# Performance work log

Measured on AMD Instinct MI355X. Metric: run time of the kernel, lower is better.

Reference implementation:

```python
import jax, jax.numpy as jnp
import numpy as np

B = 65536
SEM, COL, LAT, K, NL = 768, 64, 64, 256, 3
EPS_LN = 1e-5

def layernorm(x, g, b):
    m = jnp.mean(x, axis=-1, keepdims=True)
    v = jnp.mean((x - m) ** 2, axis=-1, keepdims=True)
    return (x - m) * jax.lax.rsqrt(v + EPS_LN) * g + b

def l2norm(x):
    n = jnp.sqrt(jnp.sum(x * x, axis=-1, keepdims=True))
    return x / jnp.maximum(n, 1e-12)

def setup_inputs() -> dict:
    key = jax.random.key(0)
    ks = jax.random.split(key, 32)
    g = lambda i, shape, s=0.02: jax.random.normal(ks[i], shape, jnp.float32) * s
    inp = {
        'semantic_emb': jax.random.normal(ks[0], (B, SEM), jnp.float32),
        'collab_emb':   jax.random.normal(ks[1], (B, COL), jnp.float32),
        # gate network: Linear(64,128)+LN+ReLU+Linear(128,64)+Sigmoid
        'gate_w1': g(2, (COL, 128)), 'gate_b1': jnp.zeros((128,)),
        'gate_ln_g': jnp.ones((128,)), 'gate_ln_b': jnp.zeros((128,)),
        'gate_w2': g(3, (128, COL)), 'gate_b2': jnp.zeros((COL,)),
        # fusion layernorm over 832
        'fusion_ln_g': jnp.ones((SEM + COL,)), 'fusion_ln_b': jnp.zeros((SEM + COL,)),
        # encoder (no bias): 832->512->256->128->64, SiLU between
        'enc_w1': g(4, (SEM + COL, 512)), 'enc_w2': g(5, (512, 256)),
        'enc_w3': g(6, (256, 128)),       'enc_w4': g(7, (128, LAT)),
        # shared decoder (no bias): 64->128->256->512, SiLU after each
        'dec_w1': g(8, (LAT, 128)), 'dec_w2': g(9, (128, 256)), 'dec_w3': g(10, (256, 512)),
        # semantic head: 512->1536 (+LN,ReLU) ->768
        'sem_w1': g(11, (512, 2 * SEM)), 'sem_b1': jnp.zeros((2 * SEM,)),
        'sem_ln_g': jnp.ones((2 * SEM,)), 'sem_ln_b': jnp.zeros((2 * SEM,)),
        'sem_w2': g(12, (2 * SEM, SEM)), 'sem_b2': jnp.zeros((SEM,)),
        # collab head: 512->256 (+LN,ReLU) ->64
        'col_w1': g(13, (512, 256)), 'col_b1': jnp.zeros((256,)),
        'col_ln_g': jnp.ones((256,)), 'col_ln_b': jnp.zeros((256,)),
        'col_w2': g(14, (256, COL)), 'col_b2': jnp.zeros((COL,)),
        # residual codebooks [n_layers, n_embed, latent_dim]
        'codebooks': jax.random.normal(ks[15], (NL, K, LAT), jnp.float32),
    }
    return inp

def _forward(semantic_emb, collab_emb, gate_w1, gate_b1, gate_ln_g, gate_ln_b,
             gate_w2, gate_b2, fusion_ln_g, fusion_ln_b,
             enc_w1, enc_w2, enc_w3, enc_w4, dec_w1, dec_w2, dec_w3,
             sem_w1, sem_b1, sem_ln_g, sem_ln_b, sem_w2, sem_b2,
             col_w1, col_b1, col_ln_g, col_ln_b, col_w2, col_b2, codebooks):
    # --- gated fusion (dropout inactive at eval) ---
    h = jax.nn.relu(layernorm(collab_emb @ gate_w1 + gate_b1, gate_ln_g, gate_ln_b))
    gate_values = jax.nn.sigmoid(h @ gate_w2 + gate_b2)
    denoised_collab = gate_values * collab_emb
    fused = layernorm(jnp.concatenate([semantic_emb, denoised_collab], axis=-1),
                      fusion_ln_g, fusion_ln_b)
    # --- encoder MLP ---
    z = jax.nn.silu(fused @ enc_w1)
    z = jax.nn.silu(z @ enc_w2)
    z = jax.nn.silu(z @ enc_w3)
    z = z @ enc_w4  # [B, LAT]
    # --- residual quantization (eval: nearest-neighbor, straight-through) ---
    residual = z
    z_q_total = jnp.zeros_like(z)
    cb_loss = jnp.float32(0.0)
    cm_loss = jnp.float32(0.0)
    codes_list = []
    for l in range(NL):
        residual = l2norm(residual)  # normalize_residuals=True
        cb = codebooks[l]  # [K, LAT]
        # argmin ||r - e||^2 == argmax (r.e - 0.5||e||^2)
        score = residual @ cb.T - 0.5 * jnp.sum(cb * cb, axis=-1)
        codes = jnp.argmax(score, axis=-1)  # [B]
        e = cb[codes]  # [B, LAT]
        cb_loss = cb_loss + jnp.mean((e - jax.lax.stop_gradient(residual)) ** 2)
        cm_loss = cm_loss + jnp.mean((jax.lax.stop_gradient(e) - residual) ** 2)
        z_q_layer = residual + jax.lax.stop_gradient(e - residual)  # straight-through
        z_q_total = z_q_total + z_q_layer
        residual = residual - z_q_layer
        codes_list.append(codes)
    codes = jnp.stack(codes_list, axis=1)  # [B, NL]
    # --- dual decoders ---
    s = jax.nn.silu(z_q_total @ dec_w1)
    s = jax.nn.silu(s @ dec_w2)
    s = jax.nn.silu(s @ dec_w3)  # [B, 512]
    sh = jax.nn.relu(layernorm(s @ sem_w1 + sem_b1, sem_ln_g, sem_ln_b))
    semantic_recon = sh @ sem_w2 + sem_b2
    ch = jax.nn.relu(layernorm(s @ col_w1 + col_b1, col_ln_g, col_ln_b))
    collab_recon = ch @ col_w2 + col_b2
    return semantic_recon, collab_recon, z_q_total, codes, cb_loss, cm_loss, gate_values

def reference(semantic_emb, collab_emb, gate_w1, gate_b1, gate_ln_g, gate_ln_b,
              gate_w2, gate_b2, fusion_ln_g, fusion_ln_b,
              enc_w1, enc_w2, enc_w3, enc_w4, dec_w1, dec_w2, dec_w3,
              sem_w1, sem_b1, sem_ln_g, sem_ln_b, sem_w2, sem_b2,
              col_w1, col_b1, col_ln_g, col_ln_b, col_w2, col_b2, codebooks):
    return _forward(semantic_emb, collab_emb, gate_w1, gate_b1, gate_ln_g, gate_ln_b,
                    gate_w2, gate_b2, fusion_ln_g, fusion_ln_b,
                    enc_w1, enc_w2, enc_w3, enc_w4, dec_w1, dec_w2, dec_w3,
                    sem_w1, sem_b1, sem_ln_g, sem_ln_b, sem_w2, sem_b2,
                    col_w1, col_b1, col_ln_g, col_ln_b, col_w2, col_b2, codebooks)
```

## Files before the change

### kernel.cpp

```cpp
#include <hip/hip_runtime.h>
#include <hip/hip_bf16.h>
#include <math.h>

typedef __bf16 bf16;
typedef __attribute__((ext_vector_type(8))) __bf16 v8bf;
typedef __attribute__((ext_vector_type(4))) float v4f;
typedef _Float16 f16;
typedef __attribute__((ext_vector_type(8))) _Float16 v8h;
typedef __attribute__((ext_vector_type(4))) _Float16 v4h;

__device__ __forceinline__ void xcd_swizzle(int& bm, int& bn) {
  const int nx = gridDim.x;
  const int id = blockIdx.y * nx + blockIdx.x;
  const int slot = id >> 3;
  const int row_in = slot / nx;
  const int bmi = (id & 7) * (gridDim.y >> 3) + row_in;
  const int bni = slot - row_in * nx;
  bm = bmi << 7; bn = bni << 7;
}

__device__ __forceinline__ void xcd_swizzle256(int& bm, int& bn) {
  const int nx = gridDim.x;
  const int id = blockIdx.y * nx + blockIdx.x;
  const int slot = id >> 3;
  const int row_in = slot / nx;
  const int bmi = (id & 7) * (gridDim.y >> 3) + row_in;
  const int bni = slot - row_in * nx;
  bm = bmi << 8; bn = bni << 8;
}

__global__ void wconv_t(const float* __restrict__ W, bf16* __restrict__ Wt, int Kd, int Nd) {
  int e = blockIdx.x * 256 + threadIdx.x;
  if (e < Kd * Nd) {
    int k = e / Nd, n = e - k * Nd;
    Wt[n * Kd + k] = (bf16)W[e];
  }
}

__global__ void wsplit_t(const float* __restrict__ W, f16* __restrict__ W0,
                         f16* __restrict__ W1, int Kd, int Nd) {
  int e = blockIdx.x * 256 + threadIdx.x;
  if (e < Kd * Nd) {
    int k = e / Nd, n = e - k * Nd;
    float v = W[e] * 2048.0f;
    f16 h0 = (f16)v;
    f16 h1 = (f16)(v - (float)h0);
    W0[n * Kd + k] = h0;
    W1[n * Kd + k] = h1;
  }
}

__global__ void cbt_k(const float* __restrict__ cb, float* __restrict__ cbT) {
  int e = blockIdx.x * 256 + threadIdx.x;
  if (e < 3 * 256 * 64) {
    int l = e >> 14, rem = e & 16383;
    int c = rem >> 6, d = rem & 63;
    cbT[l * 16384 + d * 256 + c] = cb[e];
  }
}

__global__ void nhn_k(const float* __restrict__ cb, float* __restrict__ nhn) {
  int l = blockIdx.x, c = threadIdx.x;
  const float* p = cb + l * 16384 + c * 64;
  double s = 0.0;
  for (int d = 0; d < 64; ++d) { double v = (double)p[d]; s += v * v; }
  nhn[l * 256 + c] = (float)(-0.5 * s);
}

template <int EPI>
__global__ __launch_bounds__(256, 2) void sgemm128(
    const float* __restrict__ A, const float* __restrict__ W,
    const float* __restrict__ bias, const float* __restrict__ lng,
    const float* __restrict__ lnb, float* __restrict__ C, int N, int Kd) {
  __shared__ float As[32][132];
  __shared__ float Bs[32][128];
  const int tid = threadIdx.x;
  const int w = tid >> 6, l = tid & 63;
  int tx, ty;
  if (EPI == 2) { tx = tid & 15; ty = tid >> 4; }
  else { tx = ((w & 1) << 3) | (l & 7); ty = ((w >> 1) << 3) | (l >> 3); }
  int bm, bn;
  xcd_swizzle(bm, bn);

  float acc[8][8];
#pragma unroll
  for (int i = 0; i < 8; ++i)
#pragma unroll
    for (int j = 0; j < 8; ++j) acc[i][j] = 0.0f;

  for (int k0 = 0; k0 < Kd; k0 += 32) {
    __syncthreads();
#pragma unroll
    for (int jj = 0; jj < 4; ++jj) {
      int p = tid + 256 * jj;
      int arow = p >> 3, aks = (p & 7) << 2;
      float4 v = *(const float4*)(A + (size_t)(bm + arow) * Kd + k0 + aks);
      As[aks][arow] = v.x; As[aks + 1][arow] = v.y;
      As[aks + 2][arow] = v.z; As[aks + 3][arow] = v.w;
      int bk = p >> 5, bns = (p & 31) << 2;
      float4 u = *(const float4*)(W + (size_t)(k0 + bk) * N + bn + bns);
      *(float4*)(&Bs[bk][bns]) = u;
    }
    __syncthreads();
    float cacc[8][8];
#pragma unroll
    for (int i = 0; i < 8; ++i)
#pragma unroll
      for (int j = 0; j < 8; ++j) cacc[i][j] = 0.0f;
#pragma unroll 4
    for (int kk = 0; kk < 32; ++kk) {
      float a[8], b[8];
#pragma unroll
      for (int i = 0; i < 8; ++i) a[i] = As[kk][ty * 8 + i];
#pragma unroll
      for (int j = 0; j < 8; ++j) b[j] = Bs[kk][tx * 8 + j];
#pragma unroll
      for (int i = 0; i < 8; ++i)
#pragma unroll
        for (int j = 0; j < 8; ++j) cacc[i][j] = fmaf(a[i], b[j], cacc[i][j]);
    }
#pragma unroll
    for (int i = 0; i < 8; ++i)
#pragma unroll
      for (int j = 0; j < 8; ++j) acc[i][j] += cacc[i][j];
  }

  const int colb = bn + tx * 8;
  if (EPI == 0) {
#pragma unroll
    for (int i = 0; i < 8; ++i) {
      int row = bm + ty * 8 + i;
      float o[8];
#pragma unroll
      for (int j = 0; j < 8; ++j) { float v = acc[i][j]; o[j] = v / (1.0f + expf(-v)); }
      *(float4*)(C + (size_t)row * N + colb) = make_float4(o[0], o[1], o[2], o[3]);
      *(float4*)(C + (size_t)row * N + colb + 4) = make_float4(o[4], o[5], o[6], o[7]);
    }
  } else if (EPI == 1) {
    float bb[8];
#pragma unroll
    for (int j = 0; j < 8; ++j) bb[j] = bias[colb + j];
#pragma unroll
    for (int i = 0; i < 8; ++i) {
      int row = bm + ty * 8 + i;
      float o[8];
#pragma unroll
      for (int j = 0; j < 8; ++j) o[j] = acc[i][j] + bb[j];
      *(float4*)(C + (size_t)row * N + colb) = make_float4(o[0], o[1], o[2], o[3]);
      *(float4*)(C + (size_t)row * N + colb + 4) = make_float4(o[4], o[5], o[6], o[7]);
    }
  } else {
    float bb[8], lg[8], lb[8];
#pragma unroll
    for (int j = 0; j < 8; ++j) { bb[j] = bias[colb + j]; lg[j] = lng[colb + j]; lb[j] = lnb[colb + j]; }
#pragma unroll
    for (int i = 0; i < 8; ++i) {
      int row = bm + ty * 8 + i;
      float v[8]; float s = 0.0f;
#pragma unroll
      for (int j = 0; j < 8; ++j) { v[j] = acc[i][j] + bb[j]; s += v[j]; }
      s += __shfl_xor(s, 1); s += __shfl_xor(s, 2); s += __shfl_xor(s, 4); s += __shfl_xor(s, 8);
      float mean = s * (1.0f / 128.0f);
      float ss = 0.0f;
#pragma unroll
      for (int j = 0; j < 8; ++j) { float t = v[j] - mean; ss += t * t; }
      ss += __shfl_xor(ss, 1); ss += __shfl_xor(ss, 2); ss += __shfl_xor(ss, 4); ss += __shfl_xor(ss, 8);
      float rs = 1.0f / sqrtf(ss * (1.0f / 128.0f) + 1e-5f);
      float o[8];
#pragma unroll
      for (int j = 0; j < 8; ++j) o[j] = fmaxf((v[j] - mean) * rs * lg[j] + lb[j], 0.0f);
      *(float4*)(C + (size_t)row * N + colb) = make_float4(o[0], o[1], o[2], o[3]);
      *(float4*)(C + (size_t)row * N + colb + 4) = make_float4(o[4], o[5], o[6], o[7]);
    }
  }
}

template <int EPI>
__global__ __launch_bounds__(256, 2) void sgemm64(
    const float* __restrict__ A, const float* __restrict__ W,
    const float* __restrict__ bias, const float* __restrict__ aux,
    float* __restrict__ C, float* __restrict__ C2, int Kd) {
  __shared__ float As[32][132];
  __shared__ float Bs[32][64];
  const int tid = threadIdx.x;
  const int tx = tid & 15, ty = tid >> 4;
  const int bm = blockIdx.x << 7;

  float acc[8][4];
#pragma unroll
  for (int i = 0; i < 8; ++i)
#pragma unroll
    for (int j = 0; j < 4; ++j) acc[i][j] = 0.0f;

  for (int k0 = 0; k0 < Kd; k0 += 32) {
    __syncthreads();
#pragma unroll
    for (int jj = 0; jj < 4; ++jj) {
      int p = tid + 256 * jj;
      int arow = p >> 3, aks = (p & 7) << 2;
      float4 v = *(const float4*)(A + (size_t)(bm + arow) * Kd + k0 + aks);
      As[aks][arow] = v.x; As[aks + 1][arow] = v.y;
      As[aks + 2][arow] = v.z; As[aks + 3][arow] = v.w;
    }
#pragma unroll
    for (int jj = 0; jj < 2; ++jj) {
      int p = tid + 256 * jj;
      int bk = p >> 4, bns = (p & 15) << 2;
      float4 u = *(const float4*)(W + (size_t)(k0 + bk) * 64 + bns);
      *(float4*)(&Bs[bk][bns]) = u;
    }
    __syncthreads();
    float cacc[8][4];
#pragma unroll
    for (int i = 0; i < 8; ++i)
#pragma unroll
      for (int j = 0; j < 4; ++j) cacc[i][j] = 0.0f;
#pragma unroll 4
    for (int kk = 0; kk < 32; ++kk) {
      float a[8], b[4];
#pragma unroll
      for (int i = 0; i < 8; ++i) a[i] = As[kk][ty * 8 + i];
#pragma unroll
      for (int j = 0; j < 4; ++j) b[j] = Bs[kk][tx * 4 + j];
#pragma unroll
      for (int i = 0; i < 8; ++i)
#pragma unroll
        for (int j = 0; j < 4; ++j) cacc[i][j] = fmaf(a[i], b[j], cacc[i][j]);
    }
#pragma unroll
    for (int i = 0; i < 8; ++i)
#pragma unroll
      for (int j = 0; j < 4; ++j) acc[i][j] += cacc[i][j];
  }

  const int colb = tx * 4;
  if (EPI == 0) {
#pragma unroll
    for (int i = 0; i < 8; ++i) {
      int row = bm + ty * 8 + i;
      float ss = 0.0f;
#pragma unroll
      for (int j = 0; j < 4; ++j) ss += acc[i][j] * acc[i][j];
      ss += __shfl_xor(ss, 1); ss += __shfl_xor(ss, 2); ss += __shfl_xor(ss, 4); ss += __shfl_xor(ss, 8);
      float nrm = fmaxf(sqrtf(ss), 1e-12f);
      *(float4*)(C + (size_t)row * 64 + colb) =
          make_float4(acc[i][0] / nrm, acc[i][1] / nrm, acc[i][2] / nrm, acc[i][3] / nrm);
    }
  } else if (EPI == 1) {
    float bb[4];
#pragma unroll
    for (int j = 0; j < 4; ++j) bb[j] = bias[colb + j];
#pragma unroll
    for (int i = 0; i < 8; ++i) {
      int row = bm + ty * 8 + i;
      *(float4*)(C + (size_t)row * 64 + colb) =
          make_float4(acc[i][0] + bb[0], acc[i][1] + bb[1], acc[i][2] + bb[2], acc[i][3] + bb[3]);
    }
  } else {
    float bb[4];
#pragma unroll
    for (int j = 0; j < 4; ++j) bb[j] = bias[colb + j];
#pragma unroll
    for (int i = 0; i < 8; ++i) {
      int row = bm + ty * 8 + i;
      float4 av = *(const float4*)(aux + (size_t)row * 64 + colb);
      float g[4];
#pragma unroll
      for (int j = 0; j < 4; ++j) g[j] = 1.0f / (1.0f + expf(-(acc[i][j] + bb[j])));
      *(float4*)(C + (size_t)row * 64 + colb) = make_float4(g[0], g[1], g[2], g[3]);
      *(float4*)(C2 + (size_t)row * 64 + colb) =
          make_float4(g[0] * av.x, g[1] * av.y, g[2] * av.z, g[3] * av.w);
    }
  }
}

__global__ __launch_bounds__(256) void fuse_ln(
    const float* __restrict__ sem, const float* __restrict__ den,
    const float* __restrict__ fg, const float* __restrict__ fb,
    f16* __restrict__ fA0, f16* __restrict__ fA1) {
  const int w = threadIdx.x >> 6, l = threadIdx.x & 63;
  float fgv[13], fbv[13];
#pragma unroll
  for (int q = 0; q < 12; ++q) { fgv[q] = fg[q * 64 + l]; fbv[q] = fb[q * 64 + l]; }
  fgv[12] = fg[768 + l]; fbv[12] = fb[768 + l];
  for (int it = 0; it < 4; ++it) {
    int r = (blockIdx.x * 4 + w) * 4 + it;
    float sv[12];
#pragma unroll
    for (int q = 0; q < 12; ++q) sv[q] = sem[(size_t)r * 768 + q * 64 + l];
    float dv = den[(size_t)r * 64 + l];
    float s = dv;
#pragma unroll
    for (int q = 0; q < 12; ++q) s += sv[q];
#pragma unroll
    for (int m = 1; m < 64; m <<= 1) s += __shfl_xor(s, m, 64);
    float mean = s * (1.0f / 832.0f);
    float t0 = dv - mean;
    float ss = t0 * t0;
#pragma unroll
    for (int q = 0; q < 12; ++q) { float t = sv[q] - mean; ss += t * t; }
#pragma unroll
    for (int m = 1; m < 64; m <<= 1) ss += __shfl_xor(ss, m, 64);
    float sc = 1.0f / sqrtf(ss * (1.0f / 832.0f) + 1e-5f);
#pragma unroll
    for (int q = 0; q < 13; ++q) {
      float y = (q < 12) ? ((sv[q] - mean) * sc * fgv[q] + fbv[q])
                         : (t0 * sc * fgv[12] + fbv[12]);
      float t = y * 256.0f;
      f16 h0 = (f16)t;
      size_t idx = (size_t)r * 832 + q * 64 + l;
      fA0[idx] = h0;
      fA1[idx] = (f16)(t - (float)h0);
    }
  }
}

template <int LAYER>
__global__ __launch_bounds__(256) void argupd(
    const float* __restrict__ scores, const float* __restrict__ cbl,
    float* __restrict__ rn, float* __restrict__ zq, float* __restrict__ codes,
    float* __restrict__ loss, bf16* __restrict__ zqb) {
  const int w = threadIdx.x >> 6, l = threadIdx.x & 63;
  const int base = (blockIdx.x * 4 + w) * 16;
  float lacc = 0.0f;
  for (int it = 0; it < 16; ++it) {
    int r = base + it;
    float4 s4 = *(const float4*)(scores + (size_t)r * 256 + l * 4);
    float bs = s4.x; int bi = l * 4;
    if (s4.y > bs) { bs = s4.y; bi = l * 4 + 1; }
    if (s4.z > bs) { bs = s4.z; bi = l * 4 + 2; }
    if (s4.w > bs) { bs = s4.w; bi = l * 4 + 3; }
#pragma unroll
    for (int m = 1; m < 64; m <<= 1) {
      float os = __shfl_xor(bs, m, 64);
      int oi = __shfl_xor(bi, m, 64);
      if (os > bs || (os == bs && oi < bi)) { bs = os; bi = oi; }
    }
    float e = cbl[bi * 64 + l];
    float rl = rn[(size_t)r * 64 + l];
    float emr = e - rl;
    float zql = rl + emr;
    lacc += emr * emr;
    if (l == 0) codes[r * 3 + LAYER] = (float)bi;
    if (LAYER == 0) {
      zq[(size_t)r * 64 + l] = zql;
    } else if (LAYER == 1) {
      zq[(size_t)r * 64 + l] += zql;
    } else {
      float tot = zq[(size_t)r * 64 + l] + zql;
      zq[(size_t)r * 64 + l] = tot;
      zqb[(size_t)r * 64 + l] = (bf16)tot;
    }
    if (LAYER < 2) {
      float rnew = rl - zql;
      float ss = rnew * rnew;
#pragma unroll
      for (int m = 1; m < 64; m <<= 1) ss += __shfl_xor(ss, m, 64);
      float nrm = fmaxf(sqrtf(ss), 1e-12f);
      rn[(size_t)r * 64 + l] = rnew / nrm;
    }
  }
#pragma unroll
  for (int m = 1; m < 64; m <<= 1) lacc += __shfl_xor(lacc, m, 64);
  if (l == 0) {
    float v = lacc * (1.0f / 4194304.0f);
    atomicAdd(loss, v);
    atomicAdd(loss + 1, v);
  }
}

typedef __attribute__((address_space(3))) void lds_void_t;
typedef __attribute__((address_space(1))) const void gbl_void_t;
__device__ __forceinline__ void gl_lds16(const void* g, void* l) {
  __builtin_amdgcn_global_load_lds((gbl_void_t*)g, (lds_void_t*)l, 16, 0, 0);
}

template <int EPI>
__global__ __launch_bounds__(256, 3) void bgemm(
    const bf16* __restrict__ A, const bf16* __restrict__ Wt,
    const float* __restrict__ bias, void* __restrict__ Cv, int N, int Kd) {
  __shared__ __align__(16) bf16 As[128 * 32];
  __shared__ __align__(16) bf16 Bs[128 * 32];
  const int tid = threadIdx.x;
  const int w = tid >> 6, l = tid & 63;
  int bm, bn;
  xcd_swizzle(bm, bn);
  const int wm = (w >> 1) << 6, wn = (w & 1) << 6;

  v4f acc[4][4];
  v4f z4 = {0.0f, 0.0f, 0.0f, 0.0f};
#pragma unroll
  for (int i = 0; i < 4; ++i)
#pragma unroll
    for (int j = 0; j < 4; ++j) acc[i][j] = z4;

  const int srow = (w << 5) + (l >> 2);
  const int skc = (l & 3) << 3;
  const bf16* ga0 = A + (size_t)(bm + srow) * Kd + skc;
  const bf16* gb0 = Wt + (size_t)(bn + srow) * Kd + skc;
  char* la0 = (char*)As + (w << 11);
  char* lb0 = (char*)Bs + (w << 11);

  for (int k0 = 0; k0 < Kd; k0 += 32) {
    __syncthreads();
    gl_lds16(ga0 + k0, la0);
    gl_lds16(ga0 + (size_t)16 * Kd + k0, la0 + 1024);
    gl_lds16(gb0 + k0, lb0);
    gl_lds16(gb0 + (size_t)16 * Kd + k0, lb0 + 1024);
    __syncthreads();
    v8bf af[4], bfr[4];
#pragma unroll
    for (int f = 0; f < 4; ++f) {
      af[f] = *(const v8bf*)(As + (wm + f * 16 + (l & 15)) * 32 + ((l >> 4) << 3));
      bfr[f] = *(const v8bf*)(Bs + (wn + f * 16 + (l & 15)) * 32 + ((l >> 4) << 3));
    }
#pragma unroll
    for (int mf = 0; mf < 4; ++mf)
#pragma unroll
      for (int nf = 0; nf < 4; ++nf)
        acc[mf][nf] = __builtin_amdgcn_mfma_f32_16x16x32_bf16(af[mf], bfr[nf], acc[mf][nf], 0, 0, 0);
  }

  const int cbase = bn + wn + (l & 15);
  float bb[4];
  if (EPI != 0) {
#pragma unroll
    for (int nf = 0; nf < 4; ++nf) bb[nf] = bias[cbase + nf * 16];
  }
#pragma unroll
  for (int mf = 0; mf < 4; ++mf) {
#pragma unroll
    for (int i = 0; i < 4; ++i) {
      int row = bm + wm + mf * 16 + ((l >> 4) << 2) + i;
#pragma unroll
      for (int nf = 0; nf < 4; ++nf) {
        int col = cbase + nf * 16;
        float v = acc[mf][nf][i];
        if (EPI == 0) {
          v = v / (1.0f + __expf(-v));
          ((bf16*)Cv)[(size_t)row * N + col] = (bf16)v;
        } else if (EPI == 1) {
          v += bb[nf];
          ((bf16*)Cv)[(size_t)row * N + col] = (bf16)v;
        } else {
          v += bb[nf];
          ((float*)Cv)[(size_t)row * N + col] = v;
        }
      }
    }
  }
}

__device__ __forceinline__ void stage_plane(const f16* __restrict__ src, int Kd,
                                            int rbase, int k0, char* base,
                                            int wid, int l) {
#pragma unroll
  for (int j = 0; j < 2; ++j) {
    int Cc = wid * 128 + j * 64 + l;
    int cc = Cc ^ ((Cc >> 3) & 3);
    gl_lds16(src + (size_t)(rbase + (cc >> 2)) * Kd + k0 + (cc & 3) * 8,
             base + wid * 2048 + j * 1024);
  }
}

__device__ __forceinline__ v8h ldsfragh(const char* base, int row, int kb) {
  int p = row * 64 + kb;
  p ^= ((p >> 7) & 3) << 4;
  return *(const v8h*)(base + p);
}

template <int EPI>
__global__ __launch_bounds__(256, 3) void hgemmp(
    const f16* __restrict__ A0, const f16* __restrict__ A1,
    const f16* __restrict__ W0, const f16* __restrict__ W1,
    f16* __restrict__ O0, f16* __restrict__ O1, float* __restrict__ Cf,
    int N, int Kd) {
  __shared__ __align__(16) char smem[32768];
  const int tid = threadIdx.x;
  const int w = tid >> 6, l = tid & 63;
  int bm, bn;
  xcd_swizzle(bm, bn);
  const int wm = (w >> 1) << 6, wn = (w & 1) << 6;
  const int kb = (l >> 4) << 4;

  char* pa0 = smem;
  char* pa1 = smem + 8192;
  char* pb0 = smem + 16384;
  char* pb1 = smem + 24576;

  v4f acc[4][4];
  v4f z4 = {0.0f, 0.0f, 0.0f, 0.0f};
#pragma unroll
  for (int i = 0; i < 4; ++i)
#pragma unroll
    for (int j = 0; j < 4; ++j) acc[i][j] = z4;

  for (int k0 = 0; k0 < Kd; k0 += 32) {
    __syncthreads();
    stage_plane(A0, Kd, bm, k0, pa0, w, l);
    stage_plane(A1, Kd, bm, k0, pa1, w, l);
    stage_plane(W0, Kd, bn, k0, pb0, w, l);
    stage_plane(W1, Kd, bn, k0, pb1, w, l);
    __syncthreads();
    v8h a0f[4], a1f[4], b0f[4], b1f[4];
#pragma unroll
    for (int f = 0; f < 4; ++f) {
      a0f[f] = ldsfragh(pa0, wm + f * 16 + (l & 15), kb);
      a1f[f] = ldsfragh(pa1, wm + f * 16 + (l & 15), kb);
      b0f[f] = ldsfragh(pb0, wn + f * 16 + (l & 15), kb);
      b1f[f] = ldsfragh(pb1, wn + f * 16 + (l & 15), kb);
    }
#pragma unroll
    for (int mf = 0; mf < 4; ++mf)
#pragma unroll
      for (int nf = 0; nf < 4; ++nf) {
        acc[mf][nf] = __builtin_amdgcn_mfma_f32_16x16x32_f16(a0f[mf], b1f[nf], acc[mf][nf], 0, 0, 0);
        acc[mf][nf] = __builtin_amdgcn_mfma_f32_16x16x32_f16(a1f[mf], b0f[nf], acc[mf][nf], 0, 0, 0);
        acc[mf][nf] = __builtin_amdgcn_mfma_f32_16x16x32_f16(a0f[mf], b0f[nf], acc[mf][nf], 0, 0, 0);
      }
  }

  const float sc = 1.0f / (256.0f * 2048.0f);
  const int cbase = bn + wn + (l & 15);
#pragma unroll
  for (int mf = 0; mf < 4; ++mf) {
#pragma unroll
    for (int i = 0; i < 4; ++i) {
      int row = bm + wm + mf * 16 + ((l >> 4) << 2) + i;
#pragma unroll
      for (int nf = 0; nf < 4; ++nf) {
        int col = cbase + nf * 16;
        float v = acc[mf][nf][i] * sc;
        v = v / (1.0f + expf(-v));
        if (EPI == 0) {
          float t = v * 256.0f;
          f16 h0 = (f16)t;
          O0[(size_t)row * N + col] = h0;
          O1[(size_t)row * N + col] = (f16)(t - (float)h0);
        } else {
          Cf[(size_t)row * N + col] = v;
        }
      }
    }
  }
}

__device__ __forceinline__ void stage_half(const bf16* __restrict__ src, int Kd,
                                           int rbase, int k0, char* hb8,
                                           int wid, int l) {
#pragma unroll
  for (int j = 0; j < 2; ++j) {
    int Cc = wid * 128 + j * 64 + l;
    int cc = Cc ^ (((Cc >> 3) & 3) << 1);
    gl_lds16(src + (size_t)(rbase + (cc >> 3)) * Kd + k0 + (cc & 7) * 8,
             hb8 + wid * 2048 + j * 1024);
  }
}

__device__ __forceinline__ v8bf ldsfrag(const char* base, int row, int kb) {
  int p = row * 128 + kb;
  p ^= ((p >> 7) & 3) << 5;
  return *(const v8bf*)(base + p);
}

__device__ __forceinline__ void rd_a(v8bf (&af)[2][4], const char* ab, int mh, int l) {
  const int rb = mh * 64 + (l & 15);
  const int kb = (l >> 4) * 16;
#pragma unroll
  for (int ks = 0; ks < 2; ++ks)
#pragma unroll
    for (int mf = 0; mf < 4; ++mf)
      af[ks][mf] = ldsfrag(ab, rb + mf * 16, ks * 64 + kb);
}

__device__ __forceinline__ void rd_b(v8bf (&bfr)[2][2], const char* bbp, int nh, int wl, int l) {
  const int rb = wl + nh * 32 + (l & 15);
  const int kb = (l >> 4) * 16;
#pragma unroll
  for (int ks = 0; ks < 2; ++ks)
#pragma unroll
    for (int nf = 0; nf < 2; ++nf)
      bfr[ks][nf] = ldsfrag(bbp, rb + nf * 16, ks * 64 + kb);
}

__device__ __forceinline__ void qmfma(v4f (&q)[4][2], const v8bf (&af)[2][4],
                                      const v8bf (&bfr)[2][2]) {
  __builtin_amdgcn_s_setprio(1);
#pragma unroll
  for (int ks = 0; ks < 2; ++ks)
#pragma unroll
    for (int mf = 0; mf < 4; ++mf)
#pragma unroll
      for (int nf = 0; nf < 2; ++nf)
        q[mf][nf] = __builtin_amdgcn_mfma_f32_16x16x32_bf16(af[ks][mf], bfr[ks][nf],
                                                            q[mf][nf], 0, 0, 0);
  __builtin_amdgcn_s_setprio(0);
}

#define PHASE_BAR() do { __builtin_amdgcn_s_barrier(); __builtin_amdgcn_sched_barrier(0); } while (0)

template <int EPI>
__global__ __launch_bounds__(512, 2) void bgemm8(
    const bf16* __restrict__ A, const bf16* __restrict__ Wt,
    const float* __restrict__ bias, void* __restrict__ Cv, int N, int Kd) {
  __shared__ __align__(16) char smem[131072];
  const int tid = threadIdx.x;
  const int wid = tid >> 6, l = tid & 63;
  int bm, bn;
  xcd_swizzle256(bm, bn);
  const int ha = wid >> 2;
  const int hbv = (wid & 3) >> 1;
  const int wl = (wid & 1) * 64;
  const int NT = Kd >> 6;

  v4f acc[2][2][4][2];
  v4f z4 = {0.0f, 0.0f, 0.0f, 0.0f};
#pragma unroll
  for (int a = 0; a < 2; ++a)
#pragma unroll
    for (int b = 0; b < 2; ++b)
#pragma unroll
      for (int c = 0; c < 4; ++c)
#pragma unroll
        for (int d = 0; d < 2; ++d) acc[a][b][c][d] = z4;

  stage_half(A,  Kd, bm,       0,  smem + 0,     wid, l);
  stage_half(A,  Kd, bm + 128, 0,  smem + 16384, wid, l);
  stage_half(Wt, Kd, bn,       0,  smem + 32768, wid, l);
  stage_half(Wt, Kd, bn + 128, 0,  smem + 49152, wid, l);
  stage_half(A,  Kd, bm,       64, smem + 65536, wid, l);
  stage_half(A,  Kd, bm + 128, 64, smem + 81920, wid, l);
  asm volatile("s_waitcnt vmcnt(4)" ::: "memory");
  PHASE_BAR();

  for (int K = 0; K < NT; ++K) {
    const int cur = K & 1;
    const char* ab = smem + cur * 65536 + ha * 16384;
    const char* bb = smem + cur * 65536 + 32768 + hbv * 16384;
    char* stB = smem + ((K + 1) & 1) * 65536 + 32768;
    char* stA = smem + cur * 65536;
    const int kB = (K + 1 < NT) ? (K + 1) << 6 : 0;
    const int kA = (K + 2 < NT) ? (K + 2) << 6 : 0;
    v8bf a0[2][4], a1[2][4], b0[2][2], b1[2][2];

    rd_a(a0, ab, 0, l);
    rd_b(b0, bb, 0, wl, l);
    stage_half(Wt, Kd, bn, kB, stB, wid, l);
    PHASE_BAR();
    qmfma(acc[0][0], a0, b0);
    PHASE_BAR();
    rd_b(b1, bb, 1, wl, l);
    stage_half(Wt, Kd, bn + 128, kB, stB + 16384, wid, l);
    PHASE_BAR();
    qmfma(acc[0][1], a0, b1);
    PHASE_BAR();
    rd_a(a1, ab, 1, l);
    PHASE_BAR();
    qmfma(acc[1][0], a1, b0);
    PHASE_BAR();
    stage_half(A, Kd, bm, kA, stA, wid, l);
    stage_half(A, Kd, bm + 128, kA, stA + 16384, wid, l);
    PHASE_BAR();
    qmfma(acc[1][1], a1, b1);
    asm volatile("s_waitcnt vmcnt(4)" ::: "memory");
    PHASE_BAR();
  }
  asm volatile("s_waitcnt vmcnt(0)" ::: "memory");

  const int r0 = bm + ha * 128 + ((l >> 4) << 2);
  const int c0 = bn + (wid & 3) * 64 + (l & 15);
  float bb4[2][2];
  if (EPI != 0) {
#pragma unroll
    for (int nh = 0; nh < 2; ++nh)
#pragma unroll
      for (int nf = 0; nf < 2; ++nf) bb4[nh][nf] = bias[c0 + nh * 32 + nf * 16];
  }
#pragma unroll
  for (int mh = 0; mh < 2; ++mh)
#pragma unroll
    for (int mf = 0; mf < 4; ++mf)
#pragma unroll
      for (int i = 0; i < 4; ++i) {
        const int row = r0 + mh * 64 + mf * 16 + i;
#pragma unroll
        for (int nh = 0; nh < 2; ++nh)
#pragma unroll
          for (int nf = 0; nf < 2; ++nf) {
            const int col = c0 + nh * 32 + nf * 16;
            float v = acc[mh][nh][mf][nf][i];
            if (EPI == 0) {
              v = v / (1.0f + __expf(-v));
              ((bf16*)Cv)[(size_t)row * N + col] = (bf16)v;
            } else if (EPI == 1) {
              v += bb4[nh][nf];
              ((bf16*)Cv)[(size_t)row * N + col] = (bf16)v;
            } else {
              v += bb4[nh][nf];
              ((float*)Cv)[(size_t)row * N + col] = v;
            }
          }
      }
}

template <int VPT, typename T>
__global__ __launch_bounds__(256) void ln_relu(T* __restrict__ x,
    const float* __restrict__ g, const float* __restrict__ b) {
  const int N = VPT * 256;
  const size_t base = (size_t)blockIdx.x * N;
  const int tid = threadIdx.x, w = tid >> 6, l = tid & 63;
  float v[VPT];
#pragma unroll
  for (int q = 0; q < VPT; ++q) v[q] = (float)x[base + q * 256 + tid];
  float s = 0.0f;
#pragma unroll
  for (int q = 0; q < VPT; ++q) s += v[q];
#pragma unroll
  for (int m = 1; m < 64; m <<= 1) s += __shfl_xor(s, m, 64);
  __shared__ float red[8];
  if (l == 0) red[w] = s;
  __syncthreads();
  float mean = (red[0] + red[1] + red[2] + red[3]) * (1.0f / N);
  float ss = 0.0f;
#pragma unroll
  for (int q = 0; q < VPT; ++q) { float t = v[q] - mean; ss += t * t; }
#pragma unroll
  for (int m = 1; m < 64; m <<= 1) ss += __shfl_xor(ss, m, 64);
  if (l == 0) red[4 + w] = ss;
  __syncthreads();
  float var = (red[4] + red[5] + red[6] + red[7]) * (1.0f / N);
  float rs = 1.0f / sqrtf(var + 1e-5f);
#pragma unroll
  for (int q = 0; q < VPT; ++q) {
    int j = q * 256 + tid;
    float y = (v[q] - mean) * rs * g[j] + b[j];
    x[base + j] = (T)fmaxf(y, 0.0f);
  }
}

extern "C" void kernel_launch(void* const* d_in, const int* in_sizes, int n_in,
                              void* d_out, int out_size, void* d_ws, size_t ws_size,
                              hipStream_t stream) {
  (void)in_sizes; (void)n_in; (void)out_size; (void)ws_size;
  const float* semI  = (const float*)d_in[0];
  const float* colI  = (const float*)d_in[1];
  const float* gw1   = (const float*)d_in[2];
  const float* gb1   = (const float*)d_in[3];
  const float* glng  = (const float*)d_in[4];
  const float* glnb  = (const float*)d_in[5];
  const float* gw2   = (const float*)d_in[6];
  const float* gb2   = (const float*)d_in[7];
  const float* fg    = (const float*)d_in[8];
  const float* fb    = (const float*)d_in[9];
  const float* ew1   = (const float*)d_in[10];
  const float* ew2   = (const float*)d_in[11];
  const float* ew3   = (const float*)d_in[12];
  const float* ew4   = (const float*)d_in[13];
  const float* dw1   = (const float*)d_in[14];
  const float* dw2   = (const float*)d_in[15];
  const float* dw3   = (const float*)d_in[16];
  const float* sw1   = (const float*)d_in[17];
  const float* sb1   = (const float*)d_in[18];
  const float* slng  = (const float*)d_in[19];
  const float* slnb  = (const float*)d_in[20];
  const float* sw2   = (const float*)d_in[21];
  const float* sb2   = (const float*)d_in[22];
  const float* cw1   = (const float*)d_in[23];
  const float* cb1   = (const float*)d_in[24];
  const float* clng  = (const float*)d_in[25];
  const float* clnb  = (const float*)d_in[26];
  const float* cw2   = (const float*)d_in[27];
  const float* cb2   = (const float*)d_in[28];
  const float* cbk   = (const float*)d_in[29];

  float* out = (float*)d_out;
  char* ws = (char*)d_ws;

  const size_t OUT_SEM = 0, OUT_COL = 50331648, OUT_ZQ = 54525952,
               OUT_CODES = 58720256, OUT_CB = 58916864, OUT_GATE = 58916866;

  bf16* dec1t = (bf16*)(ws + 0);
  bf16* dec2t = (bf16*)(ws + 16384);
  bf16* dec3t = (bf16*)(ws + 81920);
  bf16* sem1t = (bf16*)(ws + 344064);
  bf16* sem2t = (bf16*)(ws + 1916928);
  bf16* col1t = (bf16*)(ws + 4276224);
  float* cbT  = (float*)(ws + 4538368);
  float* nhn  = (float*)(ws + 4734976);
  f16* e1w0   = (f16*)(ws + 4739072);
  f16* e1w1   = (f16*)(ws + 5591040);
  f16* e2w0   = (f16*)(ws + 6443008);
  f16* e2w1   = (f16*)(ws + 6705152);
  f16* e3w0   = (f16*)(ws + 6967296);
  f16* e3w1   = (f16*)(ws + 7032832);
  const size_t WS_A = 8388608, WS_B = 226492416;
  f16* fA0 = (f16*)(ws + WS_A);
  f16* fA1 = (f16*)(ws + WS_A + 109051904);
  float* scores = (float*)(ws + WS_A);
  bf16*  semh   = (bf16*)(ws + WS_A);
  float* den = (float*)(ws + WS_B);
  float* hn  = (float*)(ws + WS_B + 16777216);
  f16* h1a = (f16*)(ws + WS_B);
  f16* h1b = (f16*)(ws + WS_B + 67108864);
  f16* h2a = (f16*)(ws + 360710144);
  f16* h2b = (f16*)(ws + 360710144 + 33554432);
  float* h3  = (float*)(ws + 427819008);
  float* rn  = (float*)(ws + 461373440);
  bf16* zqb  = (bf16*)(ws + WS_B);
  bf16* d1b  = (bf16*)(ws + WS_B + 8388608);
  bf16* d2b  = (bf16*)(ws + WS_B + 25165824);
  bf16* sb   = (bf16*)(ws + WS_B + 58720256);
  float* colh = (float*)(ws + WS_B + 125829120);

  hipMemsetAsync(out + OUT_CB, 0, 2 * sizeof(float), stream);

  wconv_t<<<(64 * 128 + 255) / 256, 256, 0, stream>>>(dw1, dec1t, 64, 128);
  wconv_t<<<(128 * 256 + 255) / 256, 256, 0, stream>>>(dw2, dec2t, 128, 256);
  wconv_t<<<(256 * 512 + 255) / 256, 256, 0, stream>>>(dw3, dec3t, 256, 512);
  wconv_t<<<(512 * 1536 + 255) / 256, 256, 0, stream>>>(sw1, sem1t, 512, 1536);
  wconv_t<<<(1536 * 768 + 255) / 256, 256, 0, stream>>>(sw2, sem2t, 1536, 768);
  wconv_t<<<(512 * 256 + 255) / 256, 256, 0, stream>>>(cw1, col1t, 512, 256);
  wsplit_t<<<(832 * 512 + 255) / 256, 256, 0, stream>>>(ew1, e1w0, e1w1, 832, 512);
  wsplit_t<<<(512 * 256 + 255) / 256, 256, 0, stream>>>(ew2, e2w0, e2w1, 512, 256);
  wsplit_t<<<(256 * 128 + 255) / 256, 256, 0, stream>>>(ew3, e3w0, e3w1, 256, 128);
  cbt_k<<<192, 256, 0, stream>>>(cbk, cbT);
  nhn_k<<<3, 256, 0, stream>>>(cbk, nhn);

  sgemm128<2><<<dim3(1, 512), 256, 0, stream>>>(colI, gw1, gb1, glng, glnb, hn, 128, 64);
  sgemm64<2><<<512, 256, 0, stream>>>(hn, gw2, gb2, colI, out + OUT_GATE, den, 128);
  fuse_ln<<<4096, 256, 0, stream>>>(semI, den, fg, fb, fA0, fA1);

  hgemmp<0><<<dim3(4, 512), 256, 0, stream>>>(fA0, fA1, e1w0, e1w1, h1a, h1b, nullptr, 512, 832);
  hgemmp<0><<<dim3(2, 512), 256, 0, stream>>>(h1a, h1b, e2w0, e2w1, h2a, h2b, nullptr, 256, 512);
  hgemmp<1><<<dim3(1, 512), 256, 0, stream>>>(h2a, h2b, e3w0, e3w1, nullptr, nullptr, h3, 128, 256);
  sgemm64<0><<<512, 256, 0, stream>>>(h3, ew4, nullptr, nullptr, rn, nullptr, 128);

  sgemm128<1><<<dim3(2, 512), 256, 0, stream>>>(rn, cbT + 0 * 16384, nhn + 0, nullptr, nullptr, scores, 256, 64);
  argupd<0><<<1024, 256, 0, stream>>>(scores, cbk + 0 * 16384, rn, out + OUT_ZQ, out + OUT_CODES, out + OUT_CB, zqb);
  sgemm128<1><<<dim3(2, 512), 256, 0, stream>>>(rn, cbT + 1 * 16384, nhn + 256, nullptr, nullptr, scores, 256, 64);
  argupd<1><<<1024, 256, 0, stream>>>(scores, cbk + 1 * 16384, rn, out + OUT_ZQ, out + OUT_CODES, out + OUT_CB, zqb);
  sgemm128<1><<<dim3(2, 512), 256, 0, stream>>>(rn, cbT + 2 * 16384, nhn + 512, nullptr, nullptr, scores, 256, 64);
  argupd<2><<<1024, 256, 0, stream>>>(scores, cbk + 2 * 16384, rn, out + OUT_ZQ, out + OUT_CODES, out + OUT_CB, zqb);

  bgemm<0><<<dim3(1, 512), 256, 0, stream>>>(zqb, dec1t, nullptr, d1b, 128, 64);
  bgemm8<0><<<dim3(1, 256), 512, 0, stream>>>(d1b, dec2t, nullptr, d2b, 256, 128);
  bgemm8<0><<<dim3(2, 256), 512, 0, stream>>>(d2b, dec3t, nullptr, sb, 512, 256);
  bgemm8<1><<<dim3(6, 256), 512, 0, stream>>>(sb, sem1t, sb1, semh, 1536, 512);
  ln_relu<6, bf16><<<65536, 256, 0, stream>>>(semh, slng, slnb);
  bgemm8<2><<<dim3(3, 256), 512, 0, stream>>>(semh, sem2t, sb2, out + OUT_SEM, 768, 1536);
  bgemm8<2><<<dim3(1, 256), 512, 0, stream>>>(sb, col1t, cb1, colh, 256, 512);
  ln_relu<1, float><<<65536, 256, 0, stream>>>(colh, clng, clnb);
  sgemm64<1><<<512, 256, 0, stream>>>(colh, cw2, cb2, nullptr, out + OUT_COL, nullptr, 256);
}
```

Baseline: 1.913 ms.

## Fuse residual quantization layers into one kernel with LDS-resident residuals

Replaces the three score-GEMM plus argmax/update kernel pairs with a single kernel. Each block keeps a 64-row residual tile and the current codebook in shared memory and runs all three layers in place. This removes the global scores buffer and the repeated residual and zq round trips, cutting six launches to one. In exchange it uses about 80KB of LDS per block, which limits occupancy to one block per CU, and it computes the scores with FP32 FMA instead of the previous GEMM kernel.

```diff
diff --git a/kernel.cpp b/kernel.cpp
--- a/kernel.cpp
+++ b/kernel.cpp
@@ -315,64 +315,140 @@
   }
 }
 
-template <int LAYER>
-__global__ __launch_bounds__(256) void argupd(
-    const float* __restrict__ scores, const float* __restrict__ cbl,
-    float* __restrict__ rn, float* __restrict__ zq, float* __restrict__ codes,
-    float* __restrict__ loss, bf16* __restrict__ zqb) {
-  const int w = threadIdx.x >> 6, l = threadIdx.x & 63;
-  const int base = (blockIdx.x * 4 + w) * 16;
-  float lacc = 0.0f;
-  for (int it = 0; it < 16; ++it) {
-    int r = base + it;
-    float4 s4 = *(const float4*)(scores + (size_t)r * 256 + l * 4);
-    float bs = s4.x; int bi = l * 4;
-    if (s4.y > bs) { bs = s4.y; bi = l * 4 + 1; }
-    if (s4.z > bs) { bs = s4.z; bi = l * 4 + 2; }
-    if (s4.w > bs) { bs = s4.w; bi = l * 4 + 3; }
-#pragma unroll
-    for (int m = 1; m < 64; m <<= 1) {
-      float os = __shfl_xor(bs, m, 64);
-      int oi = __shfl_xor(bi, m, 64);
-      if (os > bs || (os == bs && oi < bi)) { bs = os; bi = oi; }
-    }
-    float e = cbl[bi * 64 + l];
-    float rl = rn[(size_t)r * 64 + l];
-    float emr = e - rl;
-    float zql = rl + emr;
-    lacc += emr * emr;
-    if (l == 0) codes[r * 3 + LAYER] = (float)bi;
-    if (LAYER == 0) {
-      zq[(size_t)r * 64 + l] = zql;
-    } else if (LAYER == 1) {
-      zq[(size_t)r * 64 + l] += zql;
-    } else {
-      float tot = zq[(size_t)r * 64 + l] + zql;
-      zq[(size_t)r * 64 + l] = tot;
-      zqb[(size_t)r * 64 + l] = (bf16)tot;
-    }
-    if (LAYER < 2) {
-      float rnew = rl - zql;
-      float ss = rnew * rnew;
-#pragma unroll
-      for (int m = 1; m < 64; m <<= 1) ss += __shfl_xor(ss, m, 64);
-      float nrm = fmaxf(sqrtf(ss), 1e-12f);
-      rn[(size_t)r * 64 + l] = rnew / nrm;
-    }
-  }
-#pragma unroll
-  for (int m = 1; m < 64; m <<= 1) lacc += __shfl_xor(lacc, m, 64);
-  if (l == 0) {
-    float v = lacc * (1.0f / 4194304.0f);
-    atomicAdd(loss, v);
-    atomicAdd(loss + 1, v);
-  }
-}
-
 typedef __attribute__((address_space(3))) void lds_void_t;
 typedef __attribute__((address_space(1))) const void gbl_void_t;
 __device__ __forceinline__ void gl_lds16(const void* g, void* l) {
   __builtin_amdgcn_global_load_lds((gbl_void_t*)g, (lds_void_t*)l, 16, 0, 0);
+}
+
+__global__ __launch_bounds__(256, 1) void rq_all(
+    const float* __restrict__ rn_in, const float* __restrict__ cbT,
+    const float* __restrict__ nhn, const float* __restrict__ cbk,
+    float* __restrict__ zq, float* __restrict__ codes,
+    float* __restrict__ loss, bf16* __restrict__ zqb) {
+  __shared__ __align__(16) float Al[64 * 64];
+  __shared__ __align__(16) float Bl[64 * 256];
+  __shared__ int rowbi[64];
+  const int tid = threadIdx.x;
+  const int w = tid >> 6, l = tid & 63;
+  const int tx = tid & 31, ty = tid >> 5;
+  const int r0 = blockIdx.x << 6;
+
+#pragma unroll
+  for (int j = 0; j < 4; ++j) {
+    const int cb0 = (w << 6) + (j << 8);
+    gl_lds16(rn_in + (size_t)r0 * 64 + cb0 * 4 + l * 4, (char*)Al + cb0 * 16);
+  }
+
+  float zqa[16];
+#pragma unroll
+  for (int i = 0; i < 16; ++i) zqa[i] = 0.0f;
+
+  for (int L = 0; L < 3; ++L) {
+    __syncthreads();
+#pragma unroll
+    for (int j = 0; j < 16; ++j) {
+      const int cb0 = (w << 6) + (j << 8);
+      gl_lds16(cbT + L * 16384 + cb0 * 4 + l * 4, (char*)Bl + cb0 * 16);
+    }
+    float nh[8];
+#pragma unroll
+    for (int j = 0; j < 4; ++j) {
+      float2 n2 = *(const float2*)(nhn + L * 256 + j * 64 + tx * 2);
+      nh[j * 2] = n2.x; nh[j * 2 + 1] = n2.y;
+    }
+    __syncthreads();
+
+    float s0[8][8], s1[8][8];
+#pragma unroll
+    for (int i = 0; i < 8; ++i)
+#pragma unroll
+      for (int j = 0; j < 8; ++j) { s0[i][j] = 0.0f; s1[i][j] = 0.0f; }
+
+#define RQ_CHUNK(S, KB)                                                        \
+    for (int k4 = 0; k4 < 32; k4 += 4) {                                       \
+      float4 av[8];                                                            \
+      _Pragma("unroll")                                                        \
+      for (int i = 0; i < 8; ++i)                                              \
+        av[i] = *(const float4*)(Al + (ty * 8 + i) * 64 + (KB) + k4);          \
+      _Pragma("unroll")                                                        \
+      for (int kq = 0; kq < 4; ++kq) {                                         \
+        float bv[8];                                                           \
+        _Pragma("unroll")                                                      \
+        for (int j = 0; j < 4; ++j) {                                          \
+          float2 b2 = *(const float2*)(Bl + ((KB) + k4 + kq) * 256 + j * 64 + tx * 2); \
+          bv[j * 2] = b2.x; bv[j * 2 + 1] = b2.y;                              \
+        }                                                                      \
+        _Pragma("unroll")                                                      \
+        for (int i = 0; i < 8; ++i) {                                          \
+          float a_ = (&av[i].x)[kq];                                           \
+          _Pragma("unroll")                                                    \
+          for (int j = 0; j < 8; ++j) S[i][j] = fmaf(a_, bv[j], S[i][j]);      \
+        }                                                                      \
+      }                                                                        \
+    }
+    RQ_CHUNK(s0, 0)
+    RQ_CHUNK(s1, 32)
+#undef RQ_CHUNK
+
+#pragma unroll
+    for (int i = 0; i < 8; ++i) {
+      int r = ty * 8 + i;
+      float sc[8];
+#pragma unroll
+      for (int j = 0; j < 8; ++j) sc[j] = (s0[i][j] + s1[i][j]) + nh[j];
+      float bs = sc[0]; int bi = 2 * tx;
+#pragma unroll
+      for (int j = 1; j < 8; ++j) {
+        int cj = (j >> 1) * 64 + 2 * tx + (j & 1);
+        if (sc[j] > bs) { bs = sc[j]; bi = cj; }
+      }
+#pragma unroll
+      for (int m = 1; m < 32; m <<= 1) {
+        float os = __shfl_xor(bs, m, 64);
+        int oi = __shfl_xor(bi, m, 64);
+        if (os > bs || (os == bs && oi < bi)) { bs = os; bi = oi; }
+      }
+      if (tx == 0) {
+        rowbi[r] = bi;
+        codes[(size_t)(r0 + r) * 3 + L] = (float)bi;
+      }
+    }
+    __syncthreads();
+
+    float lacc = 0.0f;
+    const float* cbkL = cbk + L * 16384;
+#pragma unroll
+    for (int it = 0; it < 16; ++it) {
+      int r = w * 16 + it;
+      float rl = Al[r * 64 + l];
+      int bi = rowbi[r];
+      float e = cbkL[bi * 64 + l];
+      float emr = e - rl;
+      float zql = rl + emr;
+      lacc += emr * emr;
+      if (L == 0) zqa[it] = zql; else zqa[it] += zql;
+      if (L < 2) {
+        float rnew = rl - zql;
+        float ss = rnew * rnew;
+#pragma unroll
+        for (int m = 1; m < 64; m <<= 1) ss += __shfl_xor(ss, m, 64);
+        float nrm = fmaxf(sqrtf(ss), 1e-12f);
+        Al[r * 64 + l] = rnew / nrm;
+      } else {
+        float tot = zqa[it];
+        zq[(size_t)(r0 + r) * 64 + l] = tot;
+        zqb[(size_t)(r0 + r) * 64 + l] = (bf16)tot;
+      }
+    }
+#pragma unroll
+    for (int m = 1; m < 64; m <<= 1) lacc += __shfl_xor(lacc, m, 64);
+    if (l == 0) {
+      float v = lacc * (1.0f / 4194304.0f);
+      atomicAdd(loss, v);
+      atomicAdd(loss + 1, v);
+    }
+  }
 }
 
 template <int EPI>
@@ -796,7 +872,6 @@
   const size_t WS_A = 8388608, WS_B = 226492416;
   f16* fA0 = (f16*)(ws + WS_A);
   f16* fA1 = (f16*)(ws + WS_A + 109051904);
-  float* scores = (float*)(ws + WS_A);
   bf16*  semh   = (bf16*)(ws + WS_A);
   float* den = (float*)(ws + WS_B);
   float* hn  = (float*)(ws + WS_B + 16777216);
@@ -835,12 +910,8 @@
   hgemmp<1><<<dim3(1, 512), 256, 0, stream>>>(h2a, h2b, e3w0, e3w1, nullptr, nullptr, h3, 128, 256);
   sgemm64<0><<<512, 256, 0, stream>>>(h3, ew4, nullptr, nullptr, rn, nullptr, 128);
 
-  sgemm128<1><<<dim3(2, 512), 256, 0, stream>>>(rn, cbT + 0 * 16384, nhn + 0, nullptr, nullptr, scores, 256, 64);
-  argupd<0><<<1024, 256, 0, stream>>>(scores, cbk + 0 * 16384, rn, out + OUT_ZQ, out + OUT_CODES, out + OUT_CB, zqb);
-  sgemm128<1><<<dim3(2, 512), 256, 0, stream>>>(rn, cbT + 1 * 16384, nhn + 256, nullptr, nullptr, scores, 256, 64);
-  argupd<1><<<1024, 256, 0, stream>>>(scores, cbk + 1 * 16384, rn, out + OUT_ZQ, out + OUT_CODES, out + OUT_CB, zqb);
-  sgemm128<1><<<dim3(2, 512), 256, 0, stream>>>(rn, cbT + 2 * 16384, nhn + 512, nullptr, nullptr, scores, 256, 64);
-  argupd<2><<<1024, 256, 0, stream>>>(scores, cbk + 2 * 16384, rn, out + OUT_ZQ, out + OUT_CODES, out + OUT_CB, zqb);
+  rq_all<<<1024, 256, 0, stream>>>(rn, cbT, nhn, cbk,
+                                   out + OUT_ZQ, out + OUT_CODES, out + OUT_CB, zqb);
 
   bgemm<0><<<dim3(1, 512), 256, 0, stream>>>(zqb, dec1t, nullptr, d1b, 128, 64);
   bgemm8<0><<<dim3(1, 256), 512, 0, stream>>>(d1b, dec2t, nullptr, d2b, 256, 128);
```

Result: faster. 1.790 ms (-6.4%).
